# Optimization experiments

Hardware: AMD Instinct MI355X
Metric: run time of the kernel (lower is better)

## Reference

```python
import jax, jax.numpy as jnp
import numpy as np
import math

D_MODEL = 1024
NUM_HEADS = 16
D_K = D_MODEL // NUM_HEADS
SEQ_LEN = 2048
THETA = 10000.0


def _rope_tables(seq_len, d_k, theta):
    # inv_freq over even dims, angles repeated-interleaved to full d_k
    inv_freq = theta ** (-jnp.arange(0, d_k, 2, dtype=jnp.float32) / d_k)  # [d_k/2]
    pos = jnp.arange(seq_len, dtype=jnp.float32)                          # [s]
    angles = pos[:, None] * inv_freq[None, :]                             # [s, d_k/2]
    angles = jnp.repeat(angles, 2, axis=-1)                               # [s, d_k]
    return jnp.cos(angles), jnp.sin(angles)


def _rotate_half(x):
    # interleaved pairs: (x0,x1,x2,x3,...) -> (-x1,x0,-x3,x2,...)
    x_even = x[..., ::2]
    x_odd = x[..., 1::2]
    return jnp.stack([-x_odd, x_even], axis=-1).reshape(x.shape)


def _apply_rope(x, cos, sin):
    # x: [b, h, s, d_k]; cos/sin: [s, d_k]
    return x * cos + _rotate_half(x) * sin


def setup_inputs() -> dict:
    key = jax.random.key(0)
    ks = jax.random.split(key, 5)
    scale = 1.0 / math.sqrt(D_MODEL)
    X = jax.random.normal(ks[0], (2, SEQ_LEN, D_MODEL), dtype=jnp.float32)
    Wq = jax.random.normal(ks[1], (D_MODEL, D_MODEL), dtype=jnp.float32) * scale
    Wk = jax.random.normal(ks[2], (D_MODEL, D_MODEL), dtype=jnp.float32) * scale
    Wv = jax.random.normal(ks[3], (D_MODEL, D_MODEL), dtype=jnp.float32) * scale
    Wo = jax.random.normal(ks[4], (D_MODEL, D_MODEL), dtype=jnp.float32) * scale
    return {"X": X, "Wq": Wq, "Wk": Wk, "Wv": Wv, "Wo": Wo}


def reference(X, Wq, Wk, Wv, Wo):
    b, s, _ = X.shape
    h, dk = NUM_HEADS, D_K

    def proj(W):
        return (X @ W.T).reshape(b, s, h, dk).transpose(0, 2, 1, 3)  # [b,h,s,dk]

    q, k, v = proj(Wq), proj(Wk), proj(Wv)

    cos, sin = _rope_tables(s, dk, THETA)
    q = _apply_rope(q, cos, sin)
    k = _apply_rope(k, cos, sin)

    scores = jnp.einsum('bhid,bhjd->bhij', q, k) / math.sqrt(dk)
    causal = jnp.tril(jnp.ones((s, s), dtype=bool))
    scores = jnp.where(causal[None, None], scores, -jnp.inf)
    probs = jax.nn.softmax(scores, axis=-1)
    attended = jnp.einsum('bhij,bhjd->bhid', probs, v)               # [b,h,s,dk]

    out = attended.transpose(0, 2, 1, 3).reshape(b, s, h * dk)
    return out @ Wo.T
```

## Files before the change

### kernel.cpp

```cpp
#include <hip/hip_runtime.h>
#include <stdint.h>

#define D_MODEL 1024
#define NUM_HEADS 16
#define DK 64
#define SEQ 2048
#define BATCH 2
#define MROWS (BATCH * SEQ)
#define LOG2E 1.4426950408889634f
#define FIXM 14.0f

typedef short bf16x8 __attribute__((ext_vector_type(8)));
typedef float f32x4 __attribute__((ext_vector_type(4)));

__device__ __forceinline__ unsigned short f2bf(float f) {
    unsigned int u = __float_as_uint(f);
    u = (u + 0x7fffu + ((u >> 16) & 1u)) >> 16;
    return (unsigned short)u;
}
__device__ __forceinline__ unsigned short f2bf_trunc(float f) {
    return (unsigned short)(__float_as_uint(f) >> 16);
}
__device__ __forceinline__ float bf2f(unsigned short h) {
    return __uint_as_float(((unsigned int)h) << 16);
}
__device__ __forceinline__ void async16(const void* g, void* l) {
    __builtin_amdgcn_global_load_lds(
        (const __attribute__((address_space(1))) void*)g,
        (__attribute__((address_space(3))) void*)l, 16, 0, 0);
}
#define SWZ64(row, b) ((((row) * 8) + ((b) ^ ((row) & 7))) * 8)

__global__ void cast_all(const float4* __restrict__ X, const float4* __restrict__ Wq,
                         const float4* __restrict__ Wk, const float4* __restrict__ Wv,
                         const float4* __restrict__ Wo, ushort4* __restrict__ Xb,
                         ushort4* __restrict__ Wqkvb, ushort4* __restrict__ Wob) {
    int i = blockIdx.x * blockDim.x + threadIdx.x;
    const float4* src;
    ushort4* dst;
    int off;
    if (i < 1048576) { src = X; dst = Xb; off = i; }
    else if (i < 1310720) { src = Wq; dst = Wqkvb; off = i - 1048576; }
    else if (i < 1572864) { src = Wk; dst = Wqkvb + 262144; off = i - 1310720; }
    else if (i < 1835008) { src = Wv; dst = Wqkvb + 524288; off = i - 1572864; }
    else { src = Wo; dst = Wob; off = i - 1835008; }
    float4 v = src[off];
    ushort4 o;
    o.x = f2bf(v.x); o.y = f2bf(v.y); o.z = f2bf(v.z); o.w = f2bf(v.w);
    dst[off] = o;
}

template <int TN, int OUT_BF16>
__global__ __launch_bounds__(256) void gemm_tile(
    const unsigned short* __restrict__ A, const unsigned short* __restrict__ B,
    void* __restrict__ Cout, int M, int N, int K) {
    __shared__ unsigned short As[128 * 64];
    __shared__ unsigned short Bs[TN * 64];
    const int m0 = blockIdx.y * 128, n0 = blockIdx.x * TN;
    const int t = threadIdx.x;
    const int lane = t & 63, wave = t >> 6;
    const int mA = lane & 15, quad = lane >> 4;
    constexpr int MI = (TN == 128) ? 4 : 2;
    constexpr int NI = 4;
    const int wr = (TN == 128) ? (wave >> 1) * 64 : wave * 32;
    const int wc = (TN == 128) ? (wave & 1) * 64 : 0;

    f32x4 acc[MI][NI] = {};
    for (int k0 = 0; k0 < K; k0 += 64) {
#pragma unroll
        for (int i = 0; i < 4; ++i) {
            int ch = i * 256 + t;
            int r = ch >> 3, b = (ch & 7) ^ (r & 7);
            async16(A + (size_t)(m0 + r) * K + k0 + b * 8, (char*)As + ch * 16);
        }
#pragma unroll
        for (int i = 0; i < TN / 32; ++i) {
            int ch = i * 256 + t;
            int r = ch >> 3, b = (ch & 7) ^ (r & 7);
            async16(B + (size_t)(n0 + r) * K + k0 + b * 8, (char*)Bs + ch * 16);
        }
        __syncthreads();
#pragma unroll
        for (int kk = 0; kk < 2; ++kk) {
            bf16x8 af[MI], bfr[NI];
#pragma unroll
            for (int mi = 0; mi < MI; ++mi) {
                int rr = wr + mi * 16 + mA;
                af[mi] = *(const bf16x8*)&As[SWZ64(rr, kk * 4 + quad)];
            }
#pragma unroll
            for (int ni = 0; ni < NI; ++ni) {
                int rr = wc + ni * 16 + mA;
                bfr[ni] = *(const bf16x8*)&Bs[SWZ64(rr, kk * 4 + quad)];
            }
#pragma unroll
            for (int mi = 0; mi < MI; ++mi)
#pragma unroll
                for (int ni = 0; ni < NI; ++ni)
                    acc[mi][ni] = __builtin_amdgcn_mfma_f32_16x16x32_bf16(
                        af[mi], bfr[ni], acc[mi][ni], 0, 0, 0);
        }
        __syncthreads();
    }
#pragma unroll
    for (int mi = 0; mi < MI; ++mi)
#pragma unroll
        for (int ni = 0; ni < NI; ++ni)
#pragma unroll
            for (int r = 0; r < 4; ++r) {
                int gm = m0 + wr + mi * 16 + quad * 4 + r;
                int gn = n0 + wc + ni * 16 + mA;
                if (OUT_BF16)
                    ((unsigned short*)Cout)[(size_t)gm * N + gn] = f2bf(acc[mi][ni][r]);
                else
                    ((float*)Cout)[(size_t)gm * N + gn] = acc[mi][ni][r];
            }
}

__global__ __launch_bounds__(256) void rope_vt(const unsigned short* __restrict__ QKV,
                                               unsigned short* __restrict__ Qr,
                                               unsigned short* __restrict__ Kr,
                                               unsigned short* __restrict__ Vt) {
    __shared__ unsigned short T[64][80];
    const int bx = blockIdx.x;
    const int t = threadIdx.x;
    if (bx < 4096) {
        int tid = bx * 256 + t;
        int bs = tid >> 8;
        int p4 = tid & 255;
        int b = bs >> 11, spos = bs & 2047;
        int h = p4 >> 4, dd = (p4 & 15) * 4;
        float sn0, cs0, sn1, cs1;
        {
            float if0 = __expf(-(float)dd * (9.210340371976184f / 64.0f));
            float if1 = __expf(-(float)(dd + 2) * (9.210340371976184f / 64.0f));
            __sincosf((float)spos * if0, &sn0, &cs0);
            __sincosf((float)spos * if1, &sn1, &cs1);
        }
        size_t src = (size_t)bs * 3072 + h * 64 + dd;
        ushort4 qw = *(const ushort4*)&QKV[src];
        ushort4 kw = *(const ushort4*)&QKV[src + 1024];
        ushort4 qo_, ko_;
        float e = bf2f(qw.x), o = bf2f(qw.y);
        qo_.x = f2bf(e * cs0 - o * sn0); qo_.y = f2bf(o * cs0 + e * sn0);
        e = bf2f(qw.z); o = bf2f(qw.w);
        qo_.z = f2bf(e * cs1 - o * sn1); qo_.w = f2bf(o * cs1 + e * sn1);
        e = bf2f(kw.x); o = bf2f(kw.y);
        ko_.x = f2bf(e * cs0 - o * sn0); ko_.y = f2bf(o * cs0 + e * sn0);
        e = bf2f(kw.z); o = bf2f(kw.w);
        ko_.z = f2bf(e * cs1 - o * sn1); ko_.w = f2bf(o * cs1 + e * sn1);
        size_t qb = (((size_t)(b * NUM_HEADS + h) * SEQ + spos) * DK + dd);
        *(ushort4*)&Qr[qb] = qo_;
        *(ushort4*)&Kr[qb] = ko_;
    } else {
        int idx = bx - 4096;
        const int s0 = (idx & 31) * 64, bh = idx >> 5;
        const int b = bh >> 4, h = bh & 15;
#pragma unroll
        for (int i = 0; i < 2; ++i) {
            int ch = i * 256 + t;
            int row = ch >> 3, bc = ch & 7;
            *(int4*)&T[row][bc * 8] =
                *(const int4*)&QKV[(size_t)(b * SEQ + s0 + row) * 3072 + 2048 + h * 64 + bc * 8];
        }
        __syncthreads();
#pragma unroll
        for (int i = 0; i < 2; ++i) {
            int ch = i * 256 + t;
            int d = ch >> 3, sb = ch & 7;
            unsigned short tmp[8];
#pragma unroll
            for (int j = 0; j < 8; ++j) tmp[j] = T[sb * 8 + j][d];
            *(int4*)&Vt[(size_t)bh * DK * SEQ + (size_t)d * SEQ + s0 + sb * 8] = *(int4*)tmp;
        }
    }
}

__global__ __launch_bounds__(256, 4) void flash_attn6(
    const unsigned short* __restrict__ Qr, const unsigned short* __restrict__ Kr,
    const unsigned short* __restrict__ Vt, unsigned short* __restrict__ Att) {
    __shared__ unsigned short Ks[2][64 * 64];
    __shared__ unsigned short Vs[2][64 * 64];
    __shared__ unsigned short Ps[4][16 * 64];
    const int bh = blockIdx.x;
    const int qt = 31 - (int)blockIdx.y;
    const int t = threadIdx.x;
    const int lane = t & 63, wave = t >> 6;
    const int mA = lane & 15, quad = lane >> 4;
    const int qr0 = qt * 64 + wave * 16;
    const size_t qkbase = (size_t)bh * SEQ * DK;
    const unsigned short* Kg = Kr + qkbase;
    const unsigned short* Vg = Vt + (size_t)bh * DK * SEQ;

    bf16x8 aq[2];
#pragma unroll
    for (int c = 0; c < 2; ++c) {
        bf16x8 raw = *(const bf16x8*)&Qr[qkbase + (size_t)(qr0 + mA) * DK + c * 32 + quad * 8];
        bf16x8 s;
#pragma unroll
        for (int j = 0; j < 8; ++j)
            s[j] = (short)f2bf(bf2f((unsigned short)raw[j]) * (0.125f * LOG2E));
        aq[c] = s;
    }

    f32x4 accT[4] = {};
    float lsum[4] = {};

#pragma unroll
    for (int i = 0; i < 2; ++i) {
        int ch = i * 256 + t;
        int row = ch >> 3, sb = (ch & 7) ^ (row & 7);
        async16(Kg + (size_t)row * DK + sb * 8, (char*)Ks[0] + ch * 16);
        async16(Vg + (size_t)row * SEQ + sb * 8, (char*)Vs[0] + ch * 16);
    }

    for (int jt = 0; jt <= qt; ++jt) {
        __syncthreads();
        const int cur = jt & 1;
        if (jt < qt) {
            const int j1 = (jt + 1) * 64;
#pragma unroll
            for (int i = 0; i < 2; ++i) {
                int ch = i * 256 + t;
                int row = ch >> 3, sb = (ch & 7) ^ (row & 7);
                async16(Kg + (size_t)(j1 + row) * DK + sb * 8, (char*)Ks[cur ^ 1] + ch * 16);
                async16(Vg + (size_t)row * SEQ + j1 + sb * 8, (char*)Vs[cur ^ 1] + ch * 16);
            }
        }
        const int j0 = jt * 64;
        const unsigned short* Kt = Ks[cur];
        const unsigned short* Vtile = Vs[cur];
        unsigned short* Pw = Ps[wave];

        f32x4 sc[4] = {};
#pragma unroll
        for (int js = 0; js < 4; ++js) {
            int row = js * 16 + mA;
            bf16x8 b0 = *(const bf16x8*)&Kt[SWZ64(row, quad)];
            bf16x8 b1 = *(const bf16x8*)&Kt[SWZ64(row, quad + 4)];
            sc[js] = __builtin_amdgcn_mfma_f32_16x16x32_bf16(aq[0], b0, sc[js], 0, 0, 0);
            sc[js] = __builtin_amdgcn_mfma_f32_16x16x32_bf16(aq[1], b1, sc[js], 0, 0, 0);
        }
        if (jt == qt) {
#pragma unroll
            for (int js = 0; js < 4; ++js) {
                int gcol = j0 + js * 16 + mA;
#pragma unroll
                for (int r = 0; r < 4; ++r)
                    if (gcol > qr0 + quad * 4 + r) sc[js][r] = -1e30f;
            }
        }

#pragma unroll
        for (int js = 0; js < 4; ++js)
#pragma unroll
            for (int r = 0; r < 4; ++r) {
                float p = __builtin_amdgcn_exp2f(sc[js][r] - FIXM);
                lsum[r] += p;
                int q = quad * 4 + r;
                Pw[SWZ64(q, js * 2 + (mA >> 3)) + (mA & 7)] = f2bf_trunc(p);
            }
        bf16x8 ap0 = *(const bf16x8*)&Pw[SWZ64(mA, quad)];
        bf16x8 ap1 = *(const bf16x8*)&Pw[SWZ64(mA, quad + 4)];
#pragma unroll
        for (int tn = 0; tn < 4; ++tn) {
            int row = tn * 16 + mA;
            bf16x8 bv0 = *(const bf16x8*)&Vtile[SWZ64(row, quad)];
            bf16x8 bv1 = *(const bf16x8*)&Vtile[SWZ64(row, quad + 4)];
            accT[tn] = __builtin_amdgcn_mfma_f32_16x16x32_bf16(bv0, ap0, accT[tn], 0, 0, 0);
            accT[tn] = __builtin_amdgcn_mfma_f32_16x16x32_bf16(bv1, ap1, accT[tn], 0, 0, 0);
        }
    }

#pragma unroll
    for (int r = 0; r < 4; ++r)
#pragma unroll
        for (int off = 1; off < 16; off <<= 1)
            lsum[r] += __shfl_xor(lsum[r], off, 64);
    __syncthreads();
    float* LL = (float*)Ks;
    if (mA == 0)
#pragma unroll
        for (int r = 0; r < 4; ++r) LL[wave * 16 + quad * 4 + r] = lsum[r];
    __syncthreads();
    const float rl = 1.0f / LL[wave * 16 + mA];

    const int b = bh >> 4, h = bh & 15;
#pragma unroll
    for (int tn = 0; tn < 4; ++tn) {
        ushort4 o;
        o.x = f2bf(accT[tn][0] * rl);
        o.y = f2bf(accT[tn][1] * rl);
        o.z = f2bf(accT[tn][2] * rl);
        o.w = f2bf(accT[tn][3] * rl);
        *(ushort4*)&Att[(size_t)(b * SEQ + qr0 + mA) * D_MODEL + h * DK + tn * 16 + quad * 4] = o;
    }
}

extern "C" void kernel_launch(void* const* d_in, const int* in_sizes, int n_in,
                              void* d_out, int out_size, void* d_ws, size_t ws_size,
                              hipStream_t stream) {
    const float* X = (const float*)d_in[0];
    const float* Wq = (const float*)d_in[1];
    const float* Wk = (const float*)d_in[2];
    const float* Wv = (const float*)d_in[3];
    const float* Wo = (const float*)d_in[4];

    char* ws = (char*)d_ws;
    unsigned short* Xb     = (unsigned short*)(ws + 0);
    unsigned short* Wqkvb  = (unsigned short*)(ws + (8u << 20));
    unsigned short* Wob    = (unsigned short*)(ws + (14u << 20));
    unsigned short* QKVraw = (unsigned short*)(ws + (16u << 20));
    unsigned short* Kr     = (unsigned short*)(ws + (40u << 20));
    unsigned short* Vt     = (unsigned short*)(ws + (48u << 20));
    unsigned short* Qr     = Xb;
    unsigned short* Att    = QKVraw;

    cast_all<<<8192, 256, 0, stream>>>((const float4*)X, (const float4*)Wq,
                                       (const float4*)Wk, (const float4*)Wv,
                                       (const float4*)Wo, (ushort4*)Xb,
                                       (ushort4*)Wqkvb, (ushort4*)Wob);

    gemm_tile<128, 1><<<dim3(3072 / 128, MROWS / 128), 256, 0, stream>>>(
        Xb, Wqkvb, QKVraw, MROWS, 3072, D_MODEL);

    rope_vt<<<4096 + 1024, 256, 0, stream>>>(QKVraw, Qr, Kr, Vt);

    flash_attn6<<<dim3(BATCH * NUM_HEADS, 32), 256, 0, stream>>>(Qr, Kr, Vt, Att);

    gemm_tile<64, 0><<<dim3(D_MODEL / 64, MROWS / 128), 256, 0, stream>>>(
        Att, Wob, d_out, MROWS, D_MODEL, D_MODEL);
}
```

Measured before the change: 182.1 us.

## Load K/V fragments directly from global in flash attention with XCD-aware block mapping

The attention kernel drops the shared-memory double-buffered async K/V staging and instead has each wave load its MFMA operand fragments for K and V straight from global memory into registers. The V transpose is re-tiled into 64x64 blocks so each tile is contiguous. Blocks are remapped so that each XCD handles four heads, which is meant to keep K/V reuse within one L2. The row-sum normalization now uses shuffles instead of an LDS round trip, removing block barriers. The cost is that all four waves fetch the same K/V tiles redundantly through cache, and the loads are no longer overlapped with compute.

```diff
diff --git a/kernel.cpp b/kernel.cpp
--- a/kernel.cpp
+++ b/kernel.cpp
@@ -120,7 +120,7 @@
 __global__ __launch_bounds__(256) void rope_vt(const unsigned short* __restrict__ QKV,
                                                unsigned short* __restrict__ Qr,
                                                unsigned short* __restrict__ Kr,
-                                               unsigned short* __restrict__ Vt) {
+                                               unsigned short* __restrict__ Vtt) {
     __shared__ unsigned short T[64][80];
     const int bx = blockIdx.x;
     const int t = threadIdx.x;
@@ -164,6 +164,7 @@
                 *(const int4*)&QKV[(size_t)(b * SEQ + s0 + row) * 3072 + 2048 + h * 64 + bc * 8];
         }
         __syncthreads();
+        const size_t obase = (size_t)bh * DK * SEQ + (size_t)s0 * DK;
 #pragma unroll
         for (int i = 0; i < 2; ++i) {
             int ch = i * 256 + t;
@@ -171,26 +172,26 @@
             unsigned short tmp[8];
 #pragma unroll
             for (int j = 0; j < 8; ++j) tmp[j] = T[sb * 8 + j][d];
-            *(int4*)&Vt[(size_t)bh * DK * SEQ + (size_t)d * SEQ + s0 + sb * 8] = *(int4*)tmp;
-        }
-    }
-}
-
-__global__ __launch_bounds__(256, 4) void flash_attn6(
+            *(int4*)&Vtt[obase + (size_t)d * 64 + sb * 8] = *(int4*)tmp;
+        }
+    }
+}
+
+__global__ __launch_bounds__(256, 4) void flash_attn7(
     const unsigned short* __restrict__ Qr, const unsigned short* __restrict__ Kr,
-    const unsigned short* __restrict__ Vt, unsigned short* __restrict__ Att) {
-    __shared__ unsigned short Ks[2][64 * 64];
-    __shared__ unsigned short Vs[2][64 * 64];
+    const unsigned short* __restrict__ Vtt, unsigned short* __restrict__ Att) {
     __shared__ unsigned short Ps[4][16 * 64];
-    const int bh = blockIdx.x;
-    const int qt = 31 - (int)blockIdx.y;
+    const int id = blockIdx.x;
+    const int xcd = id & 7, within = id >> 3;
+    const int bh = xcd * 4 + (within & 3);
+    const int qt = 31 - (within >> 2);
     const int t = threadIdx.x;
     const int lane = t & 63, wave = t >> 6;
     const int mA = lane & 15, quad = lane >> 4;
     const int qr0 = qt * 64 + wave * 16;
     const size_t qkbase = (size_t)bh * SEQ * DK;
     const unsigned short* Kg = Kr + qkbase;
-    const unsigned short* Vg = Vt + (size_t)bh * DK * SEQ;
+    const unsigned short* Vg = Vtt + qkbase;
 
     bf16x8 aq[2];
 #pragma unroll
@@ -205,41 +206,27 @@
 
     f32x4 accT[4] = {};
     float lsum[4] = {};
-
-#pragma unroll
-    for (int i = 0; i < 2; ++i) {
-        int ch = i * 256 + t;
-        int row = ch >> 3, sb = (ch & 7) ^ (row & 7);
-        async16(Kg + (size_t)row * DK + sb * 8, (char*)Ks[0] + ch * 16);
-        async16(Vg + (size_t)row * SEQ + sb * 8, (char*)Vs[0] + ch * 16);
-    }
+    unsigned short* Pw = Ps[wave];
 
     for (int jt = 0; jt <= qt; ++jt) {
-        __syncthreads();
-        const int cur = jt & 1;
-        if (jt < qt) {
-            const int j1 = (jt + 1) * 64;
-#pragma unroll
-            for (int i = 0; i < 2; ++i) {
-                int ch = i * 256 + t;
-                int row = ch >> 3, sb = (ch & 7) ^ (row & 7);
-                async16(Kg + (size_t)(j1 + row) * DK + sb * 8, (char*)Ks[cur ^ 1] + ch * 16);
-                async16(Vg + (size_t)row * SEQ + j1 + sb * 8, (char*)Vs[cur ^ 1] + ch * 16);
-            }
-        }
         const int j0 = jt * 64;
-        const unsigned short* Kt = Ks[cur];
-        const unsigned short* Vtile = Vs[cur];
-        unsigned short* Pw = Ps[wave];
+        bf16x8 kf[4][2], vf[4][2];
+#pragma unroll
+        for (int js = 0; js < 4; ++js)
+#pragma unroll
+            for (int c = 0; c < 2; ++c)
+                kf[js][c] = *(const bf16x8*)&Kg[(size_t)(j0 + js * 16 + mA) * DK + c * 32 + quad * 8];
+#pragma unroll
+        for (int tn = 0; tn < 4; ++tn)
+#pragma unroll
+            for (int c = 0; c < 2; ++c)
+                vf[tn][c] = *(const bf16x8*)&Vg[(size_t)jt * 4096 + (tn * 16 + mA) * 64 + c * 32 + quad * 8];
 
         f32x4 sc[4] = {};
 #pragma unroll
         for (int js = 0; js < 4; ++js) {
-            int row = js * 16 + mA;
-            bf16x8 b0 = *(const bf16x8*)&Kt[SWZ64(row, quad)];
-            bf16x8 b1 = *(const bf16x8*)&Kt[SWZ64(row, quad + 4)];
-            sc[js] = __builtin_amdgcn_mfma_f32_16x16x32_bf16(aq[0], b0, sc[js], 0, 0, 0);
-            sc[js] = __builtin_amdgcn_mfma_f32_16x16x32_bf16(aq[1], b1, sc[js], 0, 0, 0);
+            sc[js] = __builtin_amdgcn_mfma_f32_16x16x32_bf16(aq[0], kf[js][0], sc[js], 0, 0, 0);
+            sc[js] = __builtin_amdgcn_mfma_f32_16x16x32_bf16(aq[1], kf[js][1], sc[js], 0, 0, 0);
         }
         if (jt == qt) {
 #pragma unroll
@@ -264,11 +251,8 @@
         bf16x8 ap1 = *(const bf16x8*)&Pw[SWZ64(mA, quad + 4)];
 #pragma unroll
         for (int tn = 0; tn < 4; ++tn) {
-            int row = tn * 16 + mA;
-            bf16x8 bv0 = *(const bf16x8*)&Vtile[SWZ64(row, quad)];
-            bf16x8 bv1 = *(const bf16x8*)&Vtile[SWZ64(row, quad + 4)];
-            accT[tn] = __builtin_amdgcn_mfma_f32_16x16x32_bf16(bv0, ap0, accT[tn], 0, 0, 0);
-            accT[tn] = __builtin_amdgcn_mfma_f32_16x16x32_bf16(bv1, ap1, accT[tn], 0, 0, 0);
+            accT[tn] = __builtin_amdgcn_mfma_f32_16x16x32_bf16(vf[tn][0], ap0, accT[tn], 0, 0, 0);
+            accT[tn] = __builtin_amdgcn_mfma_f32_16x16x32_bf16(vf[tn][1], ap1, accT[tn], 0, 0, 0);
         }
     }
 
@@ -277,13 +261,12 @@
 #pragma unroll
         for (int off = 1; off < 16; off <<= 1)
             lsum[r] += __shfl_xor(lsum[r], off, 64);
-    __syncthreads();
-    float* LL = (float*)Ks;
-    if (mA == 0)
-#pragma unroll
-        for (int r = 0; r < 4; ++r) LL[wave * 16 + quad * 4 + r] = lsum[r];
-    __syncthreads();
-    const float rl = 1.0f / LL[wave * 16 + mA];
+    const int srcl = (mA >> 2) << 4;
+    float s0 = __shfl(lsum[0], srcl), s1 = __shfl(lsum[1], srcl);
+    float s2 = __shfl(lsum[2], srcl), s3 = __shfl(lsum[3], srcl);
+    const int rr = mA & 3;
+    float sum = (rr == 0) ? s0 : (rr == 1) ? s1 : (rr == 2) ? s2 : s3;
+    const float rl = 1.0f / sum;
 
     const int b = bh >> 4, h = bh & 15;
 #pragma unroll
@@ -312,7 +295,7 @@
     unsigned short* Wob    = (unsigned short*)(ws + (14u << 20));
     unsigned short* QKVraw = (unsigned short*)(ws + (16u << 20));
     unsigned short* Kr     = (unsigned short*)(ws + (40u << 20));
-    unsigned short* Vt     = (unsigned short*)(ws + (48u << 20));
+    unsigned short* Vtt    = (unsigned short*)(ws + (48u << 20));
     unsigned short* Qr     = Xb;
     unsigned short* Att    = QKVraw;
 
@@ -324,9 +307,9 @@
     gemm_tile<128, 1><<<dim3(3072 / 128, MROWS / 128), 256, 0, stream>>>(
         Xb, Wqkvb, QKVraw, MROWS, 3072, D_MODEL);
 
-    rope_vt<<<4096 + 1024, 256, 0, stream>>>(QKVraw, Qr, Kr, Vt);
-
-    flash_attn6<<<dim3(BATCH * NUM_HEADS, 32), 256, 0, stream>>>(Qr, Kr, Vt, Att);
+    rope_vt<<<4096 + 1024, 256, 0, stream>>>(QKVraw, Qr, Kr, Vtt);
+
+    flash_attn7<<<1024, 256, 0, stream>>>(Qr, Kr, Vtt, Att);
 
     gemm_tile<64, 0><<<dim3(D_MODEL / 64, MROWS / 128), 256, 0, stream>>>(
         Att, Wob, d_out, MROWS, D_MODEL, D_MODEL);
```

New measurement: 283.4 us. +55.7%, slower.

## Fuse RoPE and V transpose into QKV projection GEMM epilogue

Applied to the files above, without the earlier changes.

Replaces the separate QKV GEMM plus rope_vt kernel with one GEMM whose epilogue applies RoPE to the Q/K sections, using a lane shuffle to fetch each pair partner, and writes V transposed directly. This removes the round trip of the raw QKV buffer through global memory and one kernel launch. In exchange the epilogue computes sincos per element, and Q/K stores become scattered 2-byte writes, which may cost write efficiency.

```diff
diff --git a/kernel.cpp b/kernel.cpp
--- a/kernel.cpp
+++ b/kernel.cpp
@@ -50,6 +50,95 @@
     dst[off] = o;
 }
 
+__global__ __launch_bounds__(256) void gemm_qkv_rope(
+    const unsigned short* __restrict__ A, const unsigned short* __restrict__ B,
+    unsigned short* __restrict__ Qr, unsigned short* __restrict__ Kr,
+    unsigned short* __restrict__ Vt) {
+    __shared__ unsigned short As[128 * 64];
+    __shared__ unsigned short Bs[128 * 64];
+    const int K = D_MODEL, N = 3072;
+    const int m0 = blockIdx.y * 128, n0 = blockIdx.x * 128;
+    const int t = threadIdx.x;
+    const int lane = t & 63, wave = t >> 6;
+    const int mA = lane & 15, quad = lane >> 4;
+    const int wr = (wave >> 1) * 64, wc = (wave & 1) * 64;
+
+    f32x4 acc[4][4] = {};
+    for (int k0 = 0; k0 < K; k0 += 64) {
+#pragma unroll
+        for (int i = 0; i < 4; ++i) {
+            int ch = i * 256 + t;
+            int r = ch >> 3, b = (ch & 7) ^ (r & 7);
+            async16(A + (size_t)(m0 + r) * K + k0 + b * 8, (char*)As + ch * 16);
+            async16(B + (size_t)(n0 + r) * K + k0 + b * 8, (char*)Bs + ch * 16);
+        }
+        __syncthreads();
+#pragma unroll
+        for (int kk = 0; kk < 2; ++kk) {
+            bf16x8 af[4], bfr[4];
+#pragma unroll
+            for (int mi = 0; mi < 4; ++mi) {
+                int rr = wr + mi * 16 + mA;
+                af[mi] = *(const bf16x8*)&As[SWZ64(rr, kk * 4 + quad)];
+            }
+#pragma unroll
+            for (int ni = 0; ni < 4; ++ni) {
+                int rr = wc + ni * 16 + mA;
+                bfr[ni] = *(const bf16x8*)&Bs[SWZ64(rr, kk * 4 + quad)];
+            }
+#pragma unroll
+            for (int mi = 0; mi < 4; ++mi)
+#pragma unroll
+                for (int ni = 0; ni < 4; ++ni)
+                    acc[mi][ni] = __builtin_amdgcn_mfma_f32_16x16x32_bf16(
+                        af[mi], bfr[ni], acc[mi][ni], 0, 0, 0);
+        }
+        __syncthreads();
+    }
+
+    const int sec = n0 >> 10;
+    if (sec == 2) {
+#pragma unroll
+        for (int mi = 0; mi < 4; ++mi)
+#pragma unroll
+            for (int ni = 0; ni < 4; ++ni) {
+                int gm = m0 + wr + mi * 16 + quad * 4;
+                int gn = n0 + wc + ni * 16 + mA;
+                int d = gn & 1023, h = d >> 6, dk = d & 63;
+                int b = gm >> 11, s = gm & 2047;
+                ushort4 o;
+                o.x = f2bf(acc[mi][ni][0]);
+                o.y = f2bf(acc[mi][ni][1]);
+                o.z = f2bf(acc[mi][ni][2]);
+                o.w = f2bf(acc[mi][ni][3]);
+                *(ushort4*)&Vt[((size_t)(b * NUM_HEADS + h) * DK + dk) * SEQ + s] = o;
+            }
+    } else {
+        unsigned short* Dst = (sec == 0) ? Qr : Kr;
+#pragma unroll
+        for (int ni = 0; ni < 4; ++ni) {
+            int gn = n0 + wc + ni * 16 + mA;
+            int d = gn & 1023, h = d >> 6, dk = d & 63;
+            float invf = __expf(-(float)(dk & ~1) * (9.210340371976184f / 64.0f));
+            float sgn = (dk & 1) ? 1.0f : -1.0f;
+#pragma unroll
+            for (int mi = 0; mi < 4; ++mi) {
+#pragma unroll
+                for (int r = 0; r < 4; ++r) {
+                    int gm = m0 + wr + mi * 16 + quad * 4 + r;
+                    int b = gm >> 11, s = gm & 2047;
+                    float sn, cs;
+                    __sincosf((float)s * invf, &sn, &cs);
+                    float val = acc[mi][ni][r];
+                    float par = __shfl_xor(val, 1, 64);
+                    float outv = val * cs + sgn * par * sn;
+                    Dst[((size_t)(b * NUM_HEADS + h) * SEQ + s) * DK + dk] = f2bf(outv);
+                }
+            }
+        }
+    }
+}
+
 template <int TN, int OUT_BF16>
 __global__ __launch_bounds__(256) void gemm_tile(
     const unsigned short* __restrict__ A, const unsigned short* __restrict__ B,
@@ -115,65 +204,6 @@
                 else
                     ((float*)Cout)[(size_t)gm * N + gn] = acc[mi][ni][r];
             }
-}
-
-__global__ __launch_bounds__(256) void rope_vt(const unsigned short* __restrict__ QKV,
-                                               unsigned short* __restrict__ Qr,
-                                               unsigned short* __restrict__ Kr,
-                                               unsigned short* __restrict__ Vt) {
-    __shared__ unsigned short T[64][80];
-    const int bx = blockIdx.x;
-    const int t = threadIdx.x;
-    if (bx < 4096) {
-        int tid = bx * 256 + t;
-        int bs = tid >> 8;
-        int p4 = tid & 255;
-        int b = bs >> 11, spos = bs & 2047;
-        int h = p4 >> 4, dd = (p4 & 15) * 4;
-        float sn0, cs0, sn1, cs1;
-        {
-            float if0 = __expf(-(float)dd * (9.210340371976184f / 64.0f));
-            float if1 = __expf(-(float)(dd + 2) * (9.210340371976184f / 64.0f));
-            __sincosf((float)spos * if0, &sn0, &cs0);
-            __sincosf((float)spos * if1, &sn1, &cs1);
-        }
-        size_t src = (size_t)bs * 3072 + h * 64 + dd;
-        ushort4 qw = *(const ushort4*)&QKV[src];
-        ushort4 kw = *(const ushort4*)&QKV[src + 1024];
-        ushort4 qo_, ko_;
-        float e = bf2f(qw.x), o = bf2f(qw.y);
-        qo_.x = f2bf(e * cs0 - o * sn0); qo_.y = f2bf(o * cs0 + e * sn0);
-        e = bf2f(qw.z); o = bf2f(qw.w);
-        qo_.z = f2bf(e * cs1 - o * sn1); qo_.w = f2bf(o * cs1 + e * sn1);
-        e = bf2f(kw.x); o = bf2f(kw.y);
-        ko_.x = f2bf(e * cs0 - o * sn0); ko_.y = f2bf(o * cs0 + e * sn0);
-        e = bf2f(kw.z); o = bf2f(kw.w);
-        ko_.z = f2bf(e * cs1 - o * sn1); ko_.w = f2bf(o * cs1 + e * sn1);
-        size_t qb = (((size_t)(b * NUM_HEADS + h) * SEQ + spos) * DK + dd);
-        *(ushort4*)&Qr[qb] = qo_;
-        *(ushort4*)&Kr[qb] = ko_;
-    } else {
-        int idx = bx - 4096;
-        const int s0 = (idx & 31) * 64, bh = idx >> 5;
-        const int b = bh >> 4, h = bh & 15;
-#pragma unroll
-        for (int i = 0; i < 2; ++i) {
-            int ch = i * 256 + t;
-            int row = ch >> 3, bc = ch & 7;
-            *(int4*)&T[row][bc * 8] =
-                *(const int4*)&QKV[(size_t)(b * SEQ + s0 + row) * 3072 + 2048 + h * 64 + bc * 8];
-        }
-        __syncthreads();
-#pragma unroll
-        for (int i = 0; i < 2; ++i) {
-            int ch = i * 256 + t;
-            int d = ch >> 3, sb = ch & 7;
-            unsigned short tmp[8];
-#pragma unroll
-            for (int j = 0; j < 8; ++j) tmp[j] = T[sb * 8 + j][d];
-            *(int4*)&Vt[(size_t)bh * DK * SEQ + (size_t)d * SEQ + s0 + sb * 8] = *(int4*)tmp;
-        }
-    }
 }
 
 __global__ __launch_bounds__(256, 4) void flash_attn6(
@@ -307,24 +337,21 @@
     const float* Wo = (const float*)d_in[4];
 
     char* ws = (char*)d_ws;
-    unsigned short* Xb     = (unsigned short*)(ws + 0);
-    unsigned short* Wqkvb  = (unsigned short*)(ws + (8u << 20));
-    unsigned short* Wob    = (unsigned short*)(ws + (14u << 20));
-    unsigned short* QKVraw = (unsigned short*)(ws + (16u << 20));
-    unsigned short* Kr     = (unsigned short*)(ws + (40u << 20));
-    unsigned short* Vt     = (unsigned short*)(ws + (48u << 20));
-    unsigned short* Qr     = Xb;
-    unsigned short* Att    = QKVraw;
+    unsigned short* Xb    = (unsigned short*)(ws + 0);
+    unsigned short* Wqkvb = (unsigned short*)(ws + (8u << 20));
+    unsigned short* Wob   = (unsigned short*)(ws + (14u << 20));
+    unsigned short* Qr    = (unsigned short*)(ws + (16u << 20));
+    unsigned short* Kr    = (unsigned short*)(ws + (24u << 20));
+    unsigned short* Vt    = (unsigned short*)(ws + (32u << 20));
+    unsigned short* Att   = (unsigned short*)(ws + (40u << 20));
 
     cast_all<<<8192, 256, 0, stream>>>((const float4*)X, (const float4*)Wq,
                                        (const float4*)Wk, (const float4*)Wv,
                                        (const float4*)Wo, (ushort4*)Xb,
                                        (ushort4*)Wqkvb, (ushort4*)Wob);
 
-    gemm_tile<128, 1><<<dim3(3072 / 128, MROWS / 128), 256, 0, stream>>>(
-        Xb, Wqkvb, QKVraw, MROWS, 3072, D_MODEL);
-
-    rope_vt<<<4096 + 1024, 256, 0, stream>>>(QKVraw, Qr, Kr, Vt);
+    gemm_qkv_rope<<<dim3(3072 / 128, MROWS / 128), 256, 0, stream>>>(
+        Xb, Wqkvb, Qr, Kr, Vt);
 
     flash_attn6<<<dim3(BATCH * NUM_HEADS, 32), 256, 0, stream>>>(Qr, Kr, Vt, Att);
 
```

Measured after the change: 182.6 us. About the same (+0.3%).
